# Kernel optimization log

Measured on AMD Instinct MI355X. Metric: run time of the kernel, lower is better.

The kernel has to match this reference:

```python
import jax, jax.numpy as jnp
import numpy as np
import math

# ---- constants lifted verbatim from the torch source ----
PMLX = 10; PX = 400; TX = PMLX + PX + PMLX          # txsize = 420
PMLY = 10; PY = 400; TY = PMLY + PY + PMLY          # tysize = 420
CX = TX // 2; CY = TY // 2
EPS0 = 1e-9 / 36 / math.pi
MU0 = 4 * math.pi * 1e-7
C0 = 1.0 / math.sqrt(MU0 * EPS0)
DX = 2.5e-8; DY = 2.5e-8
DT = 0.99 / C0 / math.sqrt((1.0 / DX) ** 2 + (1.0 / DY) ** 2)
EPSR_INF = 5.283
EPS_INF = EPS0 * EPSR_INF
F0 = 5.47e14; BW = 0.1 * F0
T = math.sqrt(2.0) * math.sqrt(math.log(2.0)) / (math.pi * BW)
NSTEPS = 200   # reduced from 16000 for the correctness baseline; same per-step math


def setup_inputs() -> dict:
    # Lorentz (complex-pole) silver model from param(): pole/residue -> a0,a1,b0,b1,b2
    pr, pi_ = -4.8113e12, 6.8512e13
    rr, ri = 4.9581e14, -1.511e18
    a0 = -2.0 * (pr * rr + pi_ * ri)
    a1 = 2.0 * rr
    b0 = pr * pr + pi_ * pi_
    b1 = -2.0 * pr
    b2 = 1.0
    den = b0 * DT * DT + 2 * b1 * DT + 4 * b2
    Ca = np.array([-(2 * b0 * DT * DT - 8 * b2) / den], np.float32)
    Cb = np.array([-(b0 * DT * DT - 2 * b1 * DT + 4 * b2) / den], np.float32)
    Cc = np.array([(2 * a0 * EPS0 * DT + 4 * a1 * EPS0) / den], np.float32)
    Cd = np.array([-(8 * a1 * EPS0) / den], np.float32)
    Ce = np.array([(-2 * a0 * EPS0 * DT + 4 * a1 * EPS0) / den], np.float32)
    temp1 = float(Cc[0])                       # sum over tot_pol = 1 pole
    denom = EPS_INF / DT + 0.5 * temp1
    C1 = np.full((TX + 1, TY + 1), (EPS_INF / DT) / denom, np.float32)
    C2 = np.full((TX + 1, TY + 1), 0.5 / denom, np.float32)
    Cb_dx = np.full((TX + 1, TY + 1), 1.0 / denom / DX, np.float32)
    Cb_dy = np.full((TX + 1, TY + 1), 1.0 / denom / DY, np.float32)
    dbhx = np.full((TX + 1, TY), DT / MU0 / DY, np.float32)   # Hx curl coeff
    dbhy = np.full((TX, TY + 1), DT / MU0 / DX, np.float32)   # Hy curl coeff
    # polynomial-graded PML conductivity profiles (pml_param)
    m = 4
    eta0 = 120.0 * math.pi
    smax = 0.8 * (m + 1) / (eta0 * DX)

    def prof(n, npml, off):
        k = np.arange(n, dtype=np.float64)
        dl = np.clip(npml - k - off, 0.0, None) / npml   # depth into left PML
        dr = np.clip(k + off - (n - 1 - npml), 0.0, None) / npml
        return (smax * (dl ** m + dr ** m)).astype(np.float32)

    sig_ex = prof(TX + 1, PMLX, 0.0)
    sig_ey = prof(TY + 1, PMLY, 0.0)
    sig_hx = prof(TX, PMLX, 0.5)   # H nodes on half-grid
    sig_hy = prof(TY, PMLY, 0.5)
    # Gaussian-modulated sine soft source at the grid center
    t = np.arange(NSTEPS, dtype=np.float64) * DT
    src = (np.exp(-(((t - 4 * T) / T) ** 2)) * np.sin(2 * math.pi * F0 * (t - 4 * T))).astype(np.float32)
    return {
        "src": jnp.asarray(src), "C1": jnp.asarray(C1), "C2": jnp.asarray(C2),
        "Cb_dx": jnp.asarray(Cb_dx), "Cb_dy": jnp.asarray(Cb_dy),
        "dbhx": jnp.asarray(dbhx), "dbhy": jnp.asarray(dbhy),
        "Ca": jnp.asarray(Ca), "Cb": jnp.asarray(Cb), "Cc": jnp.asarray(Cc),
        "Cd": jnp.asarray(Cd), "Ce": jnp.asarray(Ce),
        "sig_ex": jnp.asarray(sig_ex), "sig_ey": jnp.asarray(sig_ey),
        "sig_hx": jnp.asarray(sig_hx), "sig_hy": jnp.asarray(sig_hy),
        "n_steps": NSTEPS,
    }


def reference(src, C1, C2, Cb_dx, Cb_dy, dbhx, dbhy, Ca, Cb, Cc, Cd, Ce,
              sig_ex, sig_ey, sig_hx, sig_hy, n_steps):
    # PML damping factors (exponential time-stepping of the conductive loss)
    de = jnp.exp(-(sig_ex[:, None] + sig_ey[None, :]) * (DT / EPS0))     # (421,421) for Ez
    dhx = jnp.exp(-(sig_ex[:, None] + sig_hy[None, :]) * (DT / MU0))     # (421,420) for Hx
    dhy = jnp.exp(-(sig_hx[:, None] + sig_ey[None, :]) * (DT / MU0))     # (420,421) for Hy
    # PEC outer boundary mask
    mask = jnp.pad(jnp.ones((TX - 1, TY - 1), de.dtype), ((1, 1), (1, 1)))
    ca = Ca[:, None, None]; cb = Cb[:, None, None]; cc = Cc[:, None, None]
    cd = Cd[:, None, None]; ce = Ce[:, None, None]

    def step(carry, s):
        Ez, Eold, Hx, Hy, Jz, Jold = carry
        # H-field Yee updates with PML damping
        Hx = dhx * (Hx - dbhx * (Ez[:, 1:] - Ez[:, :-1]))
        Hy = dhy * (Hy + dbhy * (Ez[1:, :] - Ez[:-1, :]))
        # curls onto Ez nodes (interior), zero-padded at PEC boundary
        curlHy = jnp.pad(Hy[1:, :] - Hy[:-1, :], ((1, 1), (0, 0)))       # (421,421)
        curlHx = jnp.pad(Hx[:, 1:] - Hx[:, :-1], ((0, 0), (1, 1)))       # (421,421)
        # Lorentz ADE dispersion source term (tot_pol summed; Cc*Ez^{n+1} folded into C1/C2/Cb_*)
        Phi = jnp.sum((ca + 1.0) * Jz + cb * Jold + cd * Ez[None] + ce * Eold[None], axis=0)
        Ez_new = mask * de * (C1 * Ez + Cb_dx * curlHy - Cb_dy * curlHx - C2 * Phi)
        Ez_new = Ez_new.at[CX, CY].add(s)                                 # soft point source
        # polarization current recurrence
        Jz_new = ca * Jz + cb * Jold + cc * Ez_new[None] + cd * Ez[None] + ce * Eold[None]
        return (Ez_new, Ez, Hx, Hy, Jz_new, Jz), None

    z = jnp.zeros((TX + 1, TY + 1), src.dtype)
    init = (z, z,
            jnp.zeros((TX + 1, TY), src.dtype),
            jnp.zeros((TX, TY + 1), src.dtype),
            jnp.zeros((1, TX + 1, TY + 1), src.dtype),
            jnp.zeros((1, TX + 1, TY + 1), src.dtype))
    (Ez, _, _, _, _, _), _ = jax.lax.scan(step, init, src[:n_steps])
    return Ez
```

## Files before the change

kernel.cpp:

```cpp
#include <hip/hip_runtime.h>
#include <math.h>

#define NXr 421
#define CXr 210
#define NSTEPS_C 200

#define Bt   16
#define Kt   8
#define EXT  32
#define LROWS (EXT + 2)
#define SPITCH 36
#define NBLK 27
#define NPHASE (NSTEPS_C / Kt)

#define PP   448
#define PAD  8
#define CP   (CXr + PAD)
#define FSZ  (PP * PP)

typedef float v2f __attribute__((ext_vector_type(2)));
static __device__ __forceinline__ v2f mk2(float x, float y)
{ v2f r; r.x = x; r.y = y; return r; }

struct PParams {
    float *aEz, *aJz, *aU, *aHx, *aHy;
    float *bEz, *bJz, *bU, *bHx, *bHy;
    const float *dexP, *deyP, *aexP, *aeyP, *ahxP, *ahyP;
    const float *C1a, *C2a, *Cbdxa, *Cbdya;
    const float *Caa, *Cba, *Cca, *Cda, *Cea, *dbhxa, *dbhya;
    const float *src;
};

__global__ void init_kernel(const float* __restrict__ sig_ex,
                            const float* __restrict__ sig_ey,
                            const float* __restrict__ sig_hx,
                            const float* __restrict__ sig_hy,
                            float de_fac, float dh_fac,
                            float* __restrict__ zero_base, int n_zero,
                            float* __restrict__ dexP, float* __restrict__ deyP,
                            float* __restrict__ aexP, float* __restrict__ aeyP,
                            float* __restrict__ ahxP, float* __restrict__ ahyP)
{
    int t = blockIdx.x * blockDim.x + threadIdx.x;
    int stride = gridDim.x * blockDim.x;
    for (int k = t; k < n_zero; k += stride) zero_base[k] = 0.0f;
    if (t < PP) {
        int g = t - PAD;
        dexP[t] = (g >= 1 && g <= NXr - 2) ? expf(-sig_ex[g] * de_fac) : 0.0f;
        deyP[t] = (g >= 1 && g <= NXr - 2) ? expf(-sig_ey[g] * de_fac) : 0.0f;
        aexP[t] = (g >= 0 && g <  NXr)     ? expf(-sig_ex[g] * dh_fac) : 0.0f;
        aeyP[t] = (g >= 0 && g <  NXr)     ? expf(-sig_ey[g] * dh_fac) : 0.0f;
        ahxP[t] = (g >= 0 && g <  NXr - 1) ? expf(-sig_hx[g] * dh_fac) : 0.0f;
        ahyP[t] = (g >= 0 && g <  NXr - 1) ? expf(-sig_hy[g] * dh_fac) : 0.0f;
    }
}

__global__ __launch_bounds__(256)
void phase_kernel(PParams p, int t, int b0, float* __restrict__ out,
                  int writeOut)
{
    __shared__ __align__(16) float sEz[2][LROWS][SPITCH];

    const int tid = threadIdx.x;
    const int tj = tid & 15, ti = tid >> 4;
    const int li0 = 2 * ti, lj0 = 2 * tj;

    const int gx = (int)gridDim.x;
    int orig = (int)blockIdx.y * gx + (int)blockIdx.x;
    int nwg = gx * gx;
    int q = nwg >> 3, rr = nwg & 7;
    int xcd = orig & 7, kk = orig >> 3;
    int nid = (xcd < rr ? xcd * (q + 1) : rr * (q + 1) + (xcd - rr) * q) + kk;
    int bx = nid % gx, by = nid / gx;

    const int r0 = (bx + b0) * Bt + li0;
    const int c0 = (by + b0) * Bt + lj0;

    const float ca = p.Caa[0], cb = p.Cba[0], cc = p.Cca[0];
    const float cd = p.Cda[0], ce = p.Cea[0];
    const float ca1f = ca + 1.0f;
    const float C1f = p.C1a[0], C2f = p.C2a[0];
    const float cbdxf = p.Cbdxa[0], cbdyf = p.Cbdya[0];
    const float dbhx0 = p.dbhxa[0], dbhy0 = p.dbhya[0];

    const v2f vca1 = mk2(ca1f, ca1f), vcb = mk2(cb, cb), vcc = mk2(cc, cc);
    const v2f vcd = mk2(cd, cd), vce = mk2(ce, ce);
    const v2f vC1 = mk2(C1f, C1f), vC2 = mk2(C2f, C2f);
    const v2f vbx = mk2(cbdxf, cbdxf), vby = mk2(cbdyf, cbdyf);
    const v2f vhx = mk2(dbhx0, dbhx0), vhy = mk2(dbhy0, dbhy0);

    v2f dHx[2], dHy[2], dE[2], dHyU, srcw[2];
    float dHxL[2];
#pragma unroll
    for (int a = 0; a < 2; ++a) {
        float aex = p.aexP[r0 + a], ahxv = p.ahxP[r0 + a], dex = p.dexP[r0 + a];
        dHx[a] = mk2(aex * p.ahyP[c0], aex * p.ahyP[c0 + 1]);
        dHy[a] = mk2(ahxv * p.aeyP[c0], ahxv * p.aeyP[c0 + 1]);
        dE[a]  = mk2(dex * p.deyP[c0], dex * p.deyP[c0 + 1]);
        srcw[a] = mk2(((r0 + a == CP) && (c0 == CP)) ? 1.0f : 0.0f,
                      ((r0 + a == CP) && (c0 + 1 == CP)) ? 1.0f : 0.0f);
    }
    {
        float ahxU = (r0 > 0) ? p.ahxP[r0 - 1] : 0.0f;
        float ahyL = (c0 > 0) ? p.ahyP[c0 - 1] : 0.0f;
        dHyU = mk2(ahxU * p.aeyP[c0], ahxU * p.aeyP[c0 + 1]);
        dHxL[0] = p.aexP[r0] * ahyL;
        dHxL[1] = p.aexP[r0 + 1] * ahyL;
    }

    const bool odd = (t & 1) != 0;
    const float* cEz = odd ? p.bEz : p.aEz;
    const float* cJz = odd ? p.bJz : p.aJz;
    const float* cU  = odd ? p.bU  : p.aU;
    const float* cHx = odd ? p.bHx : p.aHx;
    const float* cHy = odd ? p.bHy : p.aHy;
    float* nEz = odd ? p.aEz : p.bEz;
    float* nJz = odd ? p.aJz : p.bJz;
    float* nU  = odd ? p.aU  : p.bU;
    float* nHx = odd ? p.aHx : p.bHx;
    float* nHy = odd ? p.aHy : p.bHy;

    {
        float* sp = &sEz[0][0][0];
        for (int z = tid; z < 2 * LROWS * SPITCH; z += 256) sp[z] = 0.0f;
    }

    v2f ez[2], jz[2], uu[2], hx[2], hy[2];
#pragma unroll
    for (int a = 0; a < 2; ++a) {
        int g = (r0 + a) * PP + c0;
        float2 v;
        v = *(const float2*)&cEz[g]; ez[a] = mk2(v.x, v.y);
        v = *(const float2*)&cJz[g]; jz[a] = mk2(v.x, v.y);
        v = *(const float2*)&cU[g];  uu[a] = mk2(v.x, v.y);
        v = *(const float2*)&cHx[g]; hx[a] = mk2(v.x, v.y);
        v = *(const float2*)&cHy[g]; hy[a] = mk2(v.x, v.y);
    }
    v2f hyU;
    float hxL[2];
    {
        float2 v = *(const float2*)&cHy[(r0 - 1) * PP + c0];
        hyU = mk2(v.x, v.y);
        hxL[0] = cHx[r0 * PP + c0 - 1];
        hxL[1] = cHx[(r0 + 1) * PP + c0 - 1];
    }

    const int n0 = t * Kt;
    float svl[Kt];
#pragma unroll
    for (int s = 0; s < Kt; ++s) svl[s] = p.src[n0 + s];

    __syncthreads();

    for (int s = 0; s < Kt; ++s) {
        float (*S)[SPITCH] = sEz[s & 1];
        *(float2*)&S[1 + li0][2 + lj0] = make_float2(ez[0].x, ez[0].y);
        *(float2*)&S[2 + li0][2 + lj0] = make_float2(ez[1].x, ez[1].y);

        hy[0] = dHy[0] * (hy[0] + vhy * (ez[1] - ez[0]));
        v2f w0 = hx[0] + vhx * ez[0];
        v2f w1 = hx[1] + vhx * ez[1];

        v2f phi0 = vca1 * jz[0] + vcd * ez[0] + uu[0];
        v2f phi1 = vca1 * jz[1] + vcd * ez[1] + uu[1];
        v2f base0 = vC1 * ez[0] - vC2 * phi0;
        v2f base1 = vC1 * ez[1] - vC2 * phi1;
        v2f pj0 = phi0 - jz[0];
        v2f pj1 = phi1 - jz[1];
        uu[0] = vcb * jz[0] + vce * ez[0];
        uu[1] = vcb * jz[1] + vce * ez[1];

        __syncthreads();

        float eR0 = S[1 + li0][4 + lj0];
        float eR1 = S[2 + li0][4 + lj0];
        float2 eDf = *(float2*)&S[3 + li0][2 + lj0];
        float2 eUf = *(float2*)&S[li0][2 + lj0];
        float eL0 = S[1 + li0][1 + lj0];
        float eL1 = S[2 + li0][1 + lj0];
        v2f eD = mk2(eDf.x, eDf.y), eU = mk2(eUf.x, eUf.y);

        v2f sh0 = mk2(ez[0].y, eR0);
        v2f sh1 = mk2(ez[1].y, eR1);
        hx[0] = dHx[0] * (w0 - vhx * sh0);
        hx[1] = dHx[1] * (w1 - vhx * sh1);
        hy[1] = dHy[1] * (hy[1] + vhy * (eD - ez[1]));

        hyU = dHyU * (hyU + vhy * (ez[0] - eU));
        hxL[0] = dHxL[0] * (hxL[0] - dbhx0 * (ez[0].x - eL0));
        hxL[1] = dHxL[1] * (hxL[1] - dbhx0 * (ez[1].x - eL1));

        v2f cHy0 = hy[0] - hyU;
        v2f cHy1 = hy[1] - hy[0];
        v2f cHx0 = hx[0] - mk2(hxL[0], hx[0].x);
        v2f cHx1 = hx[1] - mk2(hxL[1], hx[1].x);

        float sv = svl[s];
        v2f vsv = mk2(sv, sv);
        v2f en0 = dE[0] * (base0 + vbx * cHy0 - vby * cHx0) + srcw[0] * vsv;
        v2f en1 = dE[1] * (base1 + vbx * cHy1 - vby * cHx1) + srcw[1] * vsv;
        jz[0] = pj0 + vcc * en0;
        jz[1] = pj1 + vcc * en1;
        ez[0] = en0;
        ez[1] = en1;
    }

    if (ti >= 4 && ti < 12 && tj >= 4 && tj < 12) {
#pragma unroll
        for (int a = 0; a < 2; ++a) {
            int g = (r0 + a) * PP + c0;
            *(float2*)&nEz[g] = make_float2(ez[a].x, ez[a].y);
            *(float2*)&nJz[g] = make_float2(jz[a].x, jz[a].y);
            *(float2*)&nU[g]  = make_float2(uu[a].x, uu[a].y);
            *(float2*)&nHx[g] = make_float2(hx[a].x, hx[a].y);
            *(float2*)&nHy[g] = make_float2(hy[a].x, hy[a].y);
        }
        if (writeOut) {
#pragma unroll
            for (int a = 0; a < 2; ++a) {
                int gi = r0 + a - PAD;
                if (gi < NXr) {
                    int gj = c0 - PAD;
                    if (gj < NXr)     out[gi * NXr + gj]     = ez[a].x;
                    if (gj + 1 < NXr) out[gi * NXr + gj + 1] = ez[a].y;
                }
            }
        }
    }
}

extern "C" void kernel_launch(void* const* d_in, const int* in_sizes, int n_in,
                              void* d_out, int out_size, void* d_ws, size_t ws_size,
                              hipStream_t stream)
{
    const float* src    = (const float*)d_in[0];
    const float* C1     = (const float*)d_in[1];
    const float* C2     = (const float*)d_in[2];
    const float* Cb_dx  = (const float*)d_in[3];
    const float* Cb_dy  = (const float*)d_in[4];
    const float* dbhx   = (const float*)d_in[5];
    const float* dbhy   = (const float*)d_in[6];
    const float* Ca     = (const float*)d_in[7];
    const float* Cb     = (const float*)d_in[8];
    const float* Cc     = (const float*)d_in[9];
    const float* Cd     = (const float*)d_in[10];
    const float* Ce     = (const float*)d_in[11];
    const float* sig_ex = (const float*)d_in[12];
    const float* sig_ey = (const float*)d_in[13];
    const float* sig_hx = (const float*)d_in[14];
    const float* sig_hy = (const float*)d_in[15];

    const double EPS0 = 1e-9 / 36.0 / M_PI;
    const double MU0  = 4.0 * M_PI * 1e-7;
    const double C0   = 1.0 / sqrt(MU0 * EPS0);
    const double DXd  = 2.5e-8, DYd = 2.5e-8;
    const double DT   = 0.99 / C0 / sqrt(1.0 / (DXd * DXd) + 1.0 / (DYd * DYd));
    const float de_fac = (float)(DT / EPS0);
    const float dh_fac = (float)(DT / MU0);

    float* base = (float*)d_ws;
    float* fields = base + PP;
    float* w = fields + 10 * (size_t)FSZ;
    float* dexP = w; w += PP;
    float* deyP = w; w += PP;
    float* aexP = w; w += PP;
    float* aeyP = w; w += PP;
    float* ahxP = w; w += PP;
    float* ahyP = w; w += PP;

    PParams p;
    p.aEz = fields + 0 * (size_t)FSZ;  p.aJz = fields + 1 * (size_t)FSZ;
    p.aU  = fields + 2 * (size_t)FSZ;  p.aHx = fields + 3 * (size_t)FSZ;
    p.aHy = fields + 4 * (size_t)FSZ;
    p.bEz = fields + 5 * (size_t)FSZ;  p.bJz = fields + 6 * (size_t)FSZ;
    p.bU  = fields + 7 * (size_t)FSZ;  p.bHx = fields + 8 * (size_t)FSZ;
    p.bHy = fields + 9 * (size_t)FSZ;
    p.dexP = dexP; p.deyP = deyP; p.aexP = aexP; p.aeyP = aeyP;
    p.ahxP = ahxP; p.ahyP = ahyP;
    p.C1a = C1; p.C2a = C2; p.Cbdxa = Cb_dx; p.Cbdya = Cb_dy;
    p.Caa = Ca; p.Cba = Cb; p.Cca = Cc; p.Cda = Cd; p.Cea = Ce;
    p.dbhxa = dbhx; p.dbhya = dbhy;
    p.src = src;

    init_kernel<<<512, 256, 0, stream>>>(sig_ex, sig_ey, sig_hx, sig_hy,
                                         de_fac, dh_fac,
                                         base, PP + 10 * FSZ,
                                         dexP, deyP, aexP, aeyP, ahxP, ahyP);

    dim3 blk(256);
    for (int t = 0; t < NPHASE; ++t) {
        int R  = 8 * t + 11;
        int lo = CP - R, hi = CP + R;
        int b0 = (lo - (EXT - 1)) / 16; if (b0 < 0) b0 = 0;
        int b1 = hi / 16;               if (b1 > NBLK - 1) b1 = NBLK - 1;
        dim3 g(b1 - b0 + 1, b1 - b0 + 1);
        phase_kernel<<<g, blk, 0, stream>>>(p, t, b0, (float*)d_out,
                                            (t == NPHASE - 1) ? 1 : 0);
    }
}
```

Baseline: 246.4 us.

## Seed first 32 steps in single-block kernel and zero only shared halo ring

Adds a single 1024-thread workgroup seed kernel that runs the first 32 time steps over a 64x64 region around the source entirely in shared memory and registers. It then writes the fields and starts the phase loop at phase 4, which removes four small phase-kernel launches. The phase kernel now zeroes only the halo ring of its shared tile and drops the sync after that zeroing, relying on the in-loop barrier. The seed region must cover the causal light cone of those steps, and the seed kernel runs on one CU only.

```diff
diff --git a/kernel.cpp b/kernel.cpp
--- a/kernel.cpp
+++ b/kernel.cpp
@@ -10,6 +10,7 @@
 #define EXT  32
 #define LROWS (EXT + 2)
 #define SPITCH 36
+#define RING_N (2 * SPITCH + (LROWS - 2) * 4)
 #define NBLK 27
 #define NPHASE (NSTEPS_C / Kt)
 
@@ -17,6 +18,12 @@
 #define PAD  8
 #define CP   (CXr + PAD)
 #define FSZ  (PP * PP)
+
+#define SB   (CP - 32)
+#define SEED_STEPS 32
+#define SROWS 66
+#define SPITCH2 68
+#define RING_N2 (2 * SPITCH2 + (SROWS - 2) * 4)
 
 typedef float v2f __attribute__((ext_vector_type(2)));
 static __device__ __forceinline__ v2f mk2(float x, float y)
@@ -55,6 +62,130 @@
     }
 }
 
+__global__ __launch_bounds__(1024)
+void seed_kernel(PParams p)
+{
+    __shared__ __align__(16) float sE[2][SROWS][SPITCH2];
+
+    const int tid = threadIdx.x;
+    const int tj = tid & 31, ti = tid >> 5;
+    const int li0 = 2 * ti, lj0 = 2 * tj;
+    const int r0 = SB + li0, c0 = SB + lj0;
+
+    const float ca = p.Caa[0], cb = p.Cba[0], cc = p.Cca[0];
+    const float cd = p.Cda[0], ce = p.Cea[0];
+    const float ca1f = ca + 1.0f;
+    const float C1f = p.C1a[0], C2f = p.C2a[0];
+    const float cbdxf = p.Cbdxa[0], cbdyf = p.Cbdya[0];
+    const float dbhx0 = p.dbhxa[0], dbhy0 = p.dbhya[0];
+
+    const v2f vca1 = mk2(ca1f, ca1f), vcb = mk2(cb, cb), vcc = mk2(cc, cc);
+    const v2f vcd = mk2(cd, cd), vce = mk2(ce, ce);
+    const v2f vC1 = mk2(C1f, C1f), vC2 = mk2(C2f, C2f);
+    const v2f vbx = mk2(cbdxf, cbdxf), vby = mk2(cbdyf, cbdyf);
+    const v2f vhx = mk2(dbhx0, dbhx0), vhy = mk2(dbhy0, dbhy0);
+
+    v2f dHx[2], dHy[2], dE[2], dHyU, srcw[2];
+    float dHxL[2];
+#pragma unroll
+    for (int a = 0; a < 2; ++a) {
+        float aex = p.aexP[r0 + a], ahxv = p.ahxP[r0 + a], dex = p.dexP[r0 + a];
+        dHx[a] = mk2(aex * p.ahyP[c0], aex * p.ahyP[c0 + 1]);
+        dHy[a] = mk2(ahxv * p.aeyP[c0], ahxv * p.aeyP[c0 + 1]);
+        dE[a]  = mk2(dex * p.deyP[c0], dex * p.deyP[c0 + 1]);
+        srcw[a] = mk2(((r0 + a == CP) && (c0 == CP)) ? 1.0f : 0.0f,
+                      ((r0 + a == CP) && (c0 + 1 == CP)) ? 1.0f : 0.0f);
+    }
+    {
+        float ahxU = p.ahxP[r0 - 1];
+        float ahyL = p.ahyP[c0 - 1];
+        dHyU = mk2(ahxU * p.aeyP[c0], ahxU * p.aeyP[c0 + 1]);
+        dHxL[0] = p.aexP[r0] * ahyL;
+        dHxL[1] = p.aexP[r0 + 1] * ahyL;
+    }
+
+    v2f ez[2] = {}, jz[2] = {}, uu[2] = {}, hx[2] = {}, hy[2] = {};
+    v2f hyU = {};
+    float hxL[2] = {};
+
+    for (int z = tid; z < 2 * RING_N2; z += 1024) {
+        int b = (z >= RING_N2) ? 1 : 0;
+        int r = b ? z - RING_N2 : z;
+        int row, col;
+        if (r < 2 * SPITCH2) { row = (r < SPITCH2) ? 0 : (SROWS - 1); col = r % SPITCH2; }
+        else { int rr = r - 2 * SPITCH2; row = 1 + (rr >> 2); int c = rr & 3;
+               col = (c < 2) ? c : c + 64; }
+        sE[b][row][col] = 0.0f;
+    }
+
+    float svl[SEED_STEPS];
+#pragma unroll
+    for (int s = 0; s < SEED_STEPS; ++s) svl[s] = p.src[s];
+
+    for (int s = 0; s < SEED_STEPS; ++s) {
+        float (*S)[SPITCH2] = sE[s & 1];
+        *(float2*)&S[1 + li0][2 + lj0] = make_float2(ez[0].x, ez[0].y);
+        *(float2*)&S[2 + li0][2 + lj0] = make_float2(ez[1].x, ez[1].y);
+
+        hy[0] = dHy[0] * (hy[0] + vhy * (ez[1] - ez[0]));
+        v2f w0 = hx[0] + vhx * ez[0];
+        v2f w1 = hx[1] + vhx * ez[1];
+
+        v2f phi0 = vca1 * jz[0] + vcd * ez[0] + uu[0];
+        v2f phi1 = vca1 * jz[1] + vcd * ez[1] + uu[1];
+        v2f base0 = vC1 * ez[0] - vC2 * phi0;
+        v2f base1 = vC1 * ez[1] - vC2 * phi1;
+        v2f pj0 = phi0 - jz[0];
+        v2f pj1 = phi1 - jz[1];
+        uu[0] = vcb * jz[0] + vce * ez[0];
+        uu[1] = vcb * jz[1] + vce * ez[1];
+
+        __syncthreads();
+
+        float eR0 = S[1 + li0][4 + lj0];
+        float eR1 = S[2 + li0][4 + lj0];
+        float2 eDf = *(float2*)&S[3 + li0][2 + lj0];
+        float2 eUf = *(float2*)&S[li0][2 + lj0];
+        float eL0 = S[1 + li0][1 + lj0];
+        float eL1 = S[2 + li0][1 + lj0];
+        v2f eD = mk2(eDf.x, eDf.y), eU = mk2(eUf.x, eUf.y);
+
+        v2f sh0 = mk2(ez[0].y, eR0);
+        v2f sh1 = mk2(ez[1].y, eR1);
+        hx[0] = dHx[0] * (w0 - vhx * sh0);
+        hx[1] = dHx[1] * (w1 - vhx * sh1);
+        hy[1] = dHy[1] * (hy[1] + vhy * (eD - ez[1]));
+
+        hyU = dHyU * (hyU + vhy * (ez[0] - eU));
+        hxL[0] = dHxL[0] * (hxL[0] - dbhx0 * (ez[0].x - eL0));
+        hxL[1] = dHxL[1] * (hxL[1] - dbhx0 * (ez[1].x - eL1));
+
+        v2f cHy0 = hy[0] - hyU;
+        v2f cHy1 = hy[1] - hy[0];
+        v2f cHx0 = hx[0] - mk2(hxL[0], hx[0].x);
+        v2f cHx1 = hx[1] - mk2(hxL[1], hx[1].x);
+
+        float sv = svl[s];
+        v2f vsv = mk2(sv, sv);
+        v2f en0 = dE[0] * (base0 + vbx * cHy0 - vby * cHx0) + srcw[0] * vsv;
+        v2f en1 = dE[1] * (base1 + vbx * cHy1 - vby * cHx1) + srcw[1] * vsv;
+        jz[0] = pj0 + vcc * en0;
+        jz[1] = pj1 + vcc * en1;
+        ez[0] = en0;
+        ez[1] = en1;
+    }
+
+#pragma unroll
+    for (int a = 0; a < 2; ++a) {
+        int g = (r0 + a) * PP + c0;
+        *(float2*)&p.aEz[g] = make_float2(ez[a].x, ez[a].y);
+        *(float2*)&p.aJz[g] = make_float2(jz[a].x, jz[a].y);
+        *(float2*)&p.aU[g]  = make_float2(uu[a].x, uu[a].y);
+        *(float2*)&p.aHx[g] = make_float2(hx[a].x, hx[a].y);
+        *(float2*)&p.aHy[g] = make_float2(hy[a].x, hy[a].y);
+    }
+}
+
 __global__ __launch_bounds__(256)
 void phase_kernel(PParams p, int t, int b0, float* __restrict__ out,
                   int writeOut)
@@ -120,9 +251,14 @@
     float* nHx = odd ? p.aHx : p.bHx;
     float* nHy = odd ? p.aHy : p.bHy;
 
-    {
-        float* sp = &sEz[0][0][0];
-        for (int z = tid; z < 2 * LROWS * SPITCH; z += 256) sp[z] = 0.0f;
+    for (int z = tid; z < 2 * RING_N; z += 256) {
+        int b = (z >= RING_N) ? 1 : 0;
+        int r = b ? z - RING_N : z;
+        int row, col;
+        if (r < 2 * SPITCH) { row = (r < SPITCH) ? 0 : (LROWS - 1); col = r % SPITCH; }
+        else { int rr2 = r - 2 * SPITCH; row = 1 + (rr2 >> 2); int c = rr2 & 3;
+               col = (c < 2) ? c : c + EXT; }
+        sEz[b][row][col] = 0.0f;
     }
 
     v2f ez[2], jz[2], uu[2], hx[2], hy[2];
@@ -149,8 +285,6 @@
     float svl[Kt];
 #pragma unroll
     for (int s = 0; s < Kt; ++s) svl[s] = p.src[n0 + s];
-
-    __syncthreads();
 
     for (int s = 0; s < Kt; ++s) {
         float (*S)[SPITCH] = sEz[s & 1];
@@ -287,8 +421,10 @@
                                          base, PP + 10 * FSZ,
                                          dexP, deyP, aexP, aeyP, ahxP, ahyP);
 
+    seed_kernel<<<1, 1024, 0, stream>>>(p);
+
     dim3 blk(256);
-    for (int t = 0; t < NPHASE; ++t) {
+    for (int t = 4; t < NPHASE; ++t) {
         int R  = 8 * t + 11;
         int lo = CP - R, hi = CP + R;
         int b0 = (lo - (EXT - 1)) / 16; if (b0 < 0) b0 = 0;
```

Result: no change. 245.1 us (-0.5%).

## Replace per-phase kernel launches with a persistent kernel using neighbor flag sync

Applied to the files above, without the earlier changes.

Fuses the 25 phase launches into one persistent kernel of 729 blocks. Each block waits on atomic progress flags from its 8 neighbours instead of relying on kernel boundaries. This aims to remove launch overhead and global barriers between phases, so tiles can run ahead of distant tiles. The cost is spin-wait latency and a dependence on every block being co-resident. It also adds a bounded spin guard that could silently proceed with stale data.

```diff
diff --git a/kernel.cpp b/kernel.cpp
--- a/kernel.cpp
+++ b/kernel.cpp
@@ -10,6 +10,7 @@
 #define EXT  32
 #define LROWS (EXT + 2)
 #define SPITCH 36
+#define RING_N (2 * SPITCH + (LROWS - 2) * 4)
 #define NBLK 27
 #define NPHASE (NSTEPS_C / Kt)
 
@@ -55,9 +56,8 @@
     }
 }
 
-__global__ __launch_bounds__(256)
-void phase_kernel(PParams p, int t, int b0, float* __restrict__ out,
-                  int writeOut)
+__global__ __launch_bounds__(256, 4)
+void persist_kernel(PParams p, float* __restrict__ out, int* __restrict__ flags)
 {
     __shared__ __align__(16) float sEz[2][LROWS][SPITCH];
 
@@ -65,16 +65,26 @@
     const int tj = tid & 15, ti = tid >> 4;
     const int li0 = 2 * ti, lj0 = 2 * tj;
 
-    const int gx = (int)gridDim.x;
-    int orig = (int)blockIdx.y * gx + (int)blockIdx.x;
-    int nwg = gx * gx;
+    int orig = (int)blockIdx.x;
+    const int nwg = NBLK * NBLK;
     int q = nwg >> 3, rr = nwg & 7;
-    int xcd = orig & 7, kk = orig >> 3;
-    int nid = (xcd < rr ? xcd * (q + 1) : rr * (q + 1) + (xcd - rr) * q) + kk;
-    int bx = nid % gx, by = nid / gx;
-
-    const int r0 = (bx + b0) * Bt + li0;
-    const int c0 = (by + b0) * Bt + lj0;
+    int xcd = orig & 7, kk2 = orig >> 3;
+    int nid = (xcd < rr ? xcd * (q + 1) : rr * (q + 1) + (xcd - rr) * q) + kk2;
+    const int bi = nid % NBLK, bj = nid / NBLK;
+
+    const int r0 = bi * Bt + li0;
+    const int c0 = bj * Bt + lj0;
+    const int myflag = bi * NBLK + bj;
+
+    int spin_idx = -1;
+    if (tid < 8) {
+        int dr = (tid < 3) ? -1 : ((tid < 5) ? 0 : 1);
+        int dc = (tid < 3) ? (tid - 1)
+               : ((tid == 3) ? -1 : ((tid == 4) ? 1 : (tid - 6)));
+        int ni = bi + dr, nj = bj + dc;
+        if (ni >= 0 && ni < NBLK && nj >= 0 && nj < NBLK)
+            spin_idx = ni * NBLK + nj;
+    }
 
     const float ca = p.Caa[0], cb = p.Cba[0], cc = p.Cca[0];
     const float cd = p.Cda[0], ce = p.Cea[0];
@@ -108,123 +118,157 @@
         dHxL[1] = p.aexP[r0 + 1] * ahyL;
     }
 
-    const bool odd = (t & 1) != 0;
-    const float* cEz = odd ? p.bEz : p.aEz;
-    const float* cJz = odd ? p.bJz : p.aJz;
-    const float* cU  = odd ? p.bU  : p.aU;
-    const float* cHx = odd ? p.bHx : p.aHx;
-    const float* cHy = odd ? p.bHy : p.aHy;
-    float* nEz = odd ? p.aEz : p.bEz;
-    float* nJz = odd ? p.aJz : p.bJz;
-    float* nU  = odd ? p.aU  : p.bU;
-    float* nHx = odd ? p.aHx : p.bHx;
-    float* nHy = odd ? p.aHy : p.bHy;
-
-    {
-        float* sp = &sEz[0][0][0];
-        for (int z = tid; z < 2 * LROWS * SPITCH; z += 256) sp[z] = 0.0f;
-    }
-
-    v2f ez[2], jz[2], uu[2], hx[2], hy[2];
-#pragma unroll
-    for (int a = 0; a < 2; ++a) {
-        int g = (r0 + a) * PP + c0;
-        float2 v;
-        v = *(const float2*)&cEz[g]; ez[a] = mk2(v.x, v.y);
-        v = *(const float2*)&cJz[g]; jz[a] = mk2(v.x, v.y);
-        v = *(const float2*)&cU[g];  uu[a] = mk2(v.x, v.y);
-        v = *(const float2*)&cHx[g]; hx[a] = mk2(v.x, v.y);
-        v = *(const float2*)&cHy[g]; hy[a] = mk2(v.x, v.y);
-    }
-    v2f hyU;
-    float hxL[2];
-    {
-        float2 v = *(const float2*)&cHy[(r0 - 1) * PP + c0];
-        hyU = mk2(v.x, v.y);
-        hxL[0] = cHx[r0 * PP + c0 - 1];
-        hxL[1] = cHx[(r0 + 1) * PP + c0 - 1];
-    }
-
-    const int n0 = t * Kt;
-    float svl[Kt];
-#pragma unroll
-    for (int s = 0; s < Kt; ++s) svl[s] = p.src[n0 + s];
-
-    __syncthreads();
-
-    for (int s = 0; s < Kt; ++s) {
-        float (*S)[SPITCH] = sEz[s & 1];
-        *(float2*)&S[1 + li0][2 + lj0] = make_float2(ez[0].x, ez[0].y);
-        *(float2*)&S[2 + li0][2 + lj0] = make_float2(ez[1].x, ez[1].y);
-
-        hy[0] = dHy[0] * (hy[0] + vhy * (ez[1] - ez[0]));
-        v2f w0 = hx[0] + vhx * ez[0];
-        v2f w1 = hx[1] + vhx * ez[1];
-
-        v2f phi0 = vca1 * jz[0] + vcd * ez[0] + uu[0];
-        v2f phi1 = vca1 * jz[1] + vcd * ez[1] + uu[1];
-        v2f base0 = vC1 * ez[0] - vC2 * phi0;
-        v2f base1 = vC1 * ez[1] - vC2 * phi1;
-        v2f pj0 = phi0 - jz[0];
-        v2f pj1 = phi1 - jz[1];
-        uu[0] = vcb * jz[0] + vce * ez[0];
-        uu[1] = vcb * jz[1] + vce * ez[1];
-
+    for (int z = tid; z < 2 * RING_N; z += 256) {
+        int b = (z >= RING_N) ? 1 : 0;
+        int r = b ? z - RING_N : z;
+        int row, col;
+        if (r < 2 * SPITCH) { row = (r < SPITCH) ? 0 : (LROWS - 1); col = r % SPITCH; }
+        else { int rr2 = r - 2 * SPITCH; row = 1 + (rr2 >> 2); int c = rr2 & 3;
+               col = (c < 2) ? c : c + EXT; }
+        sEz[b][row][col] = 0.0f;
+    }
+
+    for (int k = 0; k < NPHASE; ++k) {
+        int R  = 8 * k + 11;
+        int lo = CP - R, hi = CP + R;
+        int g0 = (lo - (EXT - 1)) / Bt; if (g0 < 0) g0 = 0;
+        int g1 = hi / Bt;               if (g1 > NBLK - 1) g1 = NBLK - 1;
+        const bool active = (bi >= g0 && bi <= g1 && bj >= g0 && bj <= g1);
+
+        if (spin_idx >= 0) {
+            int guard = 0;
+            while (__hip_atomic_load(&flags[spin_idx], __ATOMIC_RELAXED,
+                                     __HIP_MEMORY_SCOPE_AGENT) < k &&
+                   ++guard < (1 << 21))
+                __builtin_amdgcn_s_sleep(1);
+        }
+        if (tid == 0 && active)
+            __builtin_amdgcn_fence(__ATOMIC_ACQUIRE, "agent");
         __syncthreads();
 
-        float eR0 = S[1 + li0][4 + lj0];
-        float eR1 = S[2 + li0][4 + lj0];
-        float2 eDf = *(float2*)&S[3 + li0][2 + lj0];
-        float2 eUf = *(float2*)&S[li0][2 + lj0];
-        float eL0 = S[1 + li0][1 + lj0];
-        float eL1 = S[2 + li0][1 + lj0];
-        v2f eD = mk2(eDf.x, eDf.y), eU = mk2(eUf.x, eUf.y);
-
-        v2f sh0 = mk2(ez[0].y, eR0);
-        v2f sh1 = mk2(ez[1].y, eR1);
-        hx[0] = dHx[0] * (w0 - vhx * sh0);
-        hx[1] = dHx[1] * (w1 - vhx * sh1);
-        hy[1] = dHy[1] * (hy[1] + vhy * (eD - ez[1]));
-
-        hyU = dHyU * (hyU + vhy * (ez[0] - eU));
-        hxL[0] = dHxL[0] * (hxL[0] - dbhx0 * (ez[0].x - eL0));
-        hxL[1] = dHxL[1] * (hxL[1] - dbhx0 * (ez[1].x - eL1));
-
-        v2f cHy0 = hy[0] - hyU;
-        v2f cHy1 = hy[1] - hy[0];
-        v2f cHx0 = hx[0] - mk2(hxL[0], hx[0].x);
-        v2f cHx1 = hx[1] - mk2(hxL[1], hx[1].x);
-
-        float sv = svl[s];
-        v2f vsv = mk2(sv, sv);
-        v2f en0 = dE[0] * (base0 + vbx * cHy0 - vby * cHx0) + srcw[0] * vsv;
-        v2f en1 = dE[1] * (base1 + vbx * cHy1 - vby * cHx1) + srcw[1] * vsv;
-        jz[0] = pj0 + vcc * en0;
-        jz[1] = pj1 + vcc * en1;
-        ez[0] = en0;
-        ez[1] = en1;
-    }
-
-    if (ti >= 4 && ti < 12 && tj >= 4 && tj < 12) {
-#pragma unroll
-        for (int a = 0; a < 2; ++a) {
-            int g = (r0 + a) * PP + c0;
-            *(float2*)&nEz[g] = make_float2(ez[a].x, ez[a].y);
-            *(float2*)&nJz[g] = make_float2(jz[a].x, jz[a].y);
-            *(float2*)&nU[g]  = make_float2(uu[a].x, uu[a].y);
-            *(float2*)&nHx[g] = make_float2(hx[a].x, hx[a].y);
-            *(float2*)&nHy[g] = make_float2(hy[a].x, hy[a].y);
-        }
-        if (writeOut) {
+        if (active) {
+            const bool odd = (k & 1) != 0;
+            const float* cEz = odd ? p.bEz : p.aEz;
+            const float* cJz = odd ? p.bJz : p.aJz;
+            const float* cU  = odd ? p.bU  : p.aU;
+            const float* cHx = odd ? p.bHx : p.aHx;
+            const float* cHy = odd ? p.bHy : p.aHy;
+            float* nEz = odd ? p.aEz : p.bEz;
+            float* nJz = odd ? p.aJz : p.bJz;
+            float* nU  = odd ? p.aU  : p.bU;
+            float* nHx = odd ? p.aHx : p.bHx;
+            float* nHy = odd ? p.aHy : p.bHy;
+
+            v2f ez[2], jz[2], uu[2], hx[2], hy[2];
 #pragma unroll
             for (int a = 0; a < 2; ++a) {
-                int gi = r0 + a - PAD;
-                if (gi < NXr) {
-                    int gj = c0 - PAD;
-                    if (gj < NXr)     out[gi * NXr + gj]     = ez[a].x;
-                    if (gj + 1 < NXr) out[gi * NXr + gj + 1] = ez[a].y;
+                int g = (r0 + a) * PP + c0;
+                float2 v;
+                v = *(const float2*)&cEz[g]; ez[a] = mk2(v.x, v.y);
+                v = *(const float2*)&cJz[g]; jz[a] = mk2(v.x, v.y);
+                v = *(const float2*)&cU[g];  uu[a] = mk2(v.x, v.y);
+                v = *(const float2*)&cHx[g]; hx[a] = mk2(v.x, v.y);
+                v = *(const float2*)&cHy[g]; hy[a] = mk2(v.x, v.y);
+            }
+            v2f hyU;
+            float hxL[2];
+            {
+                float2 v = *(const float2*)&cHy[(r0 - 1) * PP + c0];
+                hyU = mk2(v.x, v.y);
+                hxL[0] = cHx[r0 * PP + c0 - 1];
+                hxL[1] = cHx[(r0 + 1) * PP + c0 - 1];
+            }
+
+            const int n0 = k * Kt;
+            float svl[Kt];
+#pragma unroll
+            for (int s = 0; s < Kt; ++s) svl[s] = p.src[n0 + s];
+
+            for (int s = 0; s < Kt; ++s) {
+                float (*S)[SPITCH] = sEz[s & 1];
+                *(float2*)&S[1 + li0][2 + lj0] = make_float2(ez[0].x, ez[0].y);
+                *(float2*)&S[2 + li0][2 + lj0] = make_float2(ez[1].x, ez[1].y);
+
+                hy[0] = dHy[0] * (hy[0] + vhy * (ez[1] - ez[0]));
+                v2f w0 = hx[0] + vhx * ez[0];
+                v2f w1 = hx[1] + vhx * ez[1];
+
+                v2f phi0 = vca1 * jz[0] + vcd * ez[0] + uu[0];
+                v2f phi1 = vca1 * jz[1] + vcd * ez[1] + uu[1];
+                v2f base0 = vC1 * ez[0] - vC2 * phi0;
+                v2f base1 = vC1 * ez[1] - vC2 * phi1;
+                v2f pj0 = phi0 - jz[0];
+                v2f pj1 = phi1 - jz[1];
+                uu[0] = vcb * jz[0] + vce * ez[0];
+                uu[1] = vcb * jz[1] + vce * ez[1];
+
+                __syncthreads();
+
+                float eR0 = S[1 + li0][4 + lj0];
+                float eR1 = S[2 + li0][4 + lj0];
+                float2 eDf = *(float2*)&S[3 + li0][2 + lj0];
+                float2 eUf = *(float2*)&S[li0][2 + lj0];
+                float eL0 = S[1 + li0][1 + lj0];
+                float eL1 = S[2 + li0][1 + lj0];
+                v2f eD = mk2(eDf.x, eDf.y), eU = mk2(eUf.x, eUf.y);
+
+                v2f sh0 = mk2(ez[0].y, eR0);
+                v2f sh1 = mk2(ez[1].y, eR1);
+                hx[0] = dHx[0] * (w0 - vhx * sh0);
+                hx[1] = dHx[1] * (w1 - vhx * sh1);
+                hy[1] = dHy[1] * (hy[1] + vhy * (eD - ez[1]));
+
+                hyU = dHyU * (hyU + vhy * (ez[0] - eU));
+                hxL[0] = dHxL[0] * (hxL[0] - dbhx0 * (ez[0].x - eL0));
+                hxL[1] = dHxL[1] * (hxL[1] - dbhx0 * (ez[1].x - eL1));
+
+                v2f cHy0 = hy[0] - hyU;
+                v2f cHy1 = hy[1] - hy[0];
+                v2f cHx0 = hx[0] - mk2(hxL[0], hx[0].x);
+                v2f cHx1 = hx[1] - mk2(hxL[1], hx[1].x);
+
+                float sv = svl[s];
+                v2f vsv = mk2(sv, sv);
+                v2f en0 = dE[0] * (base0 + vbx * cHy0 - vby * cHx0) + srcw[0] * vsv;
+                v2f en1 = dE[1] * (base1 + vbx * cHy1 - vby * cHx1) + srcw[1] * vsv;
+                jz[0] = pj0 + vcc * en0;
+                jz[1] = pj1 + vcc * en1;
+                ez[0] = en0;
+                ez[1] = en1;
+            }
+
+            if (ti >= 4 && ti < 12 && tj >= 4 && tj < 12) {
+#pragma unroll
+                for (int a = 0; a < 2; ++a) {
+                    int g = (r0 + a) * PP + c0;
+                    *(float2*)&nEz[g] = make_float2(ez[a].x, ez[a].y);
+                    *(float2*)&nJz[g] = make_float2(jz[a].x, jz[a].y);
+                    *(float2*)&nU[g]  = make_float2(uu[a].x, uu[a].y);
+                    *(float2*)&nHx[g] = make_float2(hx[a].x, hx[a].y);
+                    *(float2*)&nHy[g] = make_float2(hy[a].x, hy[a].y);
+                }
+                if (k == NPHASE - 1) {
+#pragma unroll
+                    for (int a = 0; a < 2; ++a) {
+                        int gi = r0 + a - PAD;
+                        if (gi < NXr) {
+                            int gj = c0 - PAD;
+                            if (gj < NXr)     out[gi * NXr + gj]     = ez[a].x;
+                            if (gj + 1 < NXr) out[gi * NXr + gj + 1] = ez[a].y;
+                        }
+                    }
                 }
             }
+        }
+
+        __syncthreads();
+        if (tid == 0) {
+            if (active)
+                __hip_atomic_store(&flags[myflag], k + 1, __ATOMIC_RELEASE,
+                                   __HIP_MEMORY_SCOPE_AGENT);
+            else
+                __hip_atomic_store(&flags[myflag], k + 1, __ATOMIC_RELAXED,
+                                   __HIP_MEMORY_SCOPE_AGENT);
         }
     }
 }
@@ -260,13 +304,15 @@
 
     float* base = (float*)d_ws;
     float* fields = base + PP;
-    float* w = fields + 10 * (size_t)FSZ;
+    int*   flags  = (int*)(fields + 10 * (size_t)FSZ);
+    float* w = fields + 10 * (size_t)FSZ + 768;
     float* dexP = w; w += PP;
     float* deyP = w; w += PP;
     float* aexP = w; w += PP;
     float* aeyP = w; w += PP;
     float* ahxP = w; w += PP;
     float* ahyP = w; w += PP;
+    const int n_zero = PP + 10 * FSZ + 768;
 
     PParams p;
     p.aEz = fields + 0 * (size_t)FSZ;  p.aJz = fields + 1 * (size_t)FSZ;
@@ -284,17 +330,9 @@
 
     init_kernel<<<512, 256, 0, stream>>>(sig_ex, sig_ey, sig_hx, sig_hy,
                                          de_fac, dh_fac,
-                                         base, PP + 10 * FSZ,
+                                         base, n_zero,
                                          dexP, deyP, aexP, aeyP, ahxP, ahyP);
 
-    dim3 blk(256);
-    for (int t = 0; t < NPHASE; ++t) {
-        int R  = 8 * t + 11;
-        int lo = CP - R, hi = CP + R;
-        int b0 = (lo - (EXT - 1)) / 16; if (b0 < 0) b0 = 0;
-        int b1 = hi / 16;               if (b1 > NBLK - 1) b1 = NBLK - 1;
-        dim3 g(b1 - b0 + 1, b1 - b0 + 1);
-        phase_kernel<<<g, blk, 0, stream>>>(p, t, b0, (float*)d_out,
-                                            (t == NPHASE - 1) ? 1 : 0);
-    }
+    persist_kernel<<<dim3(NBLK * NBLK), dim3(256), 0, stream>>>(
+        p, (float*)d_out, flags);
 }
```

After: 626.0 us. +154.1%, slower.
